# Performance work log

Hardware: AMD Instinct MI355X
Metric: run time of the kernel (lower is better)

## Reference

```python
import jax, jax.numpy as jnp
import numpy as np

N_HEAD, D_MODEL, D_HEAD = 16, 1024, 64
EPS = 1e-5
SCALE = 1.0 / np.sqrt(D_HEAD)


def setup_inputs() -> dict:
    key = jax.random.key(0)
    k1, k2, k3 = jax.random.split(key, 3)
    slen, bsz = 2048, 4
    h = jax.random.normal(k1, (slen, bsz, D_MODEL), dtype=jnp.float32)
    w_qkvb = jax.random.normal(k2, (N_HEAD * (3 * D_HEAD + 1), D_MODEL), dtype=jnp.float32) / np.sqrt(D_MODEL)
    w_o = jax.random.normal(k3, (D_MODEL, N_HEAD * D_HEAD), dtype=jnp.float32) / np.sqrt(N_HEAD * D_HEAD)
    ln_g = jnp.ones((D_MODEL,), dtype=jnp.float32)
    ln_b = jnp.zeros((D_MODEL,), dtype=jnp.float32)
    return {"h": h, "w_qkvb": w_qkvb, "w_o": w_o, "ln_g": ln_g, "ln_b": ln_b}


def _layer_norm(x, g, b):
    mu = jnp.mean(x, axis=-1, keepdims=True)
    var = jnp.mean(jnp.square(x - mu), axis=-1, keepdims=True)
    return (x - mu) * jax.lax.rsqrt(var + EPS) * g + b


def _fast_weight_memory(q, k, v, beta):
    # q,k,v: [b,h,l,d]; beta: [b,h,l,1]. Delta-rule recurrence over l.
    b, hn, l, d = q.shape
    qs = jnp.moveaxis(q, 2, 0)      # [l,b,h,d]
    ks = jnp.moveaxis(k, 2, 0)
    vs = jnp.moveaxis(v, 2, 0)
    bs = jnp.moveaxis(beta, 2, 0)   # [l,b,h,1]

    def step(W, xs):
        qt, kt, vt, bt = xs
        v_old = jnp.einsum('bhij,bhj->bhi', W, kt)
        delta = bt * (vt - v_old)                     # [b,h,d]
        W = W + delta[..., :, None] * kt[..., None, :]
        out = jnp.einsum('bhij,bhj->bhi', W, qt)
        return W, out

    W0 = jnp.zeros((b, hn, d, d), dtype=q.dtype)
    _, outs = jax.lax.scan(step, W0, (qs, ks, vs, bs))
    return jnp.moveaxis(outs, 0, 2)  # [b,h,l,d]


def reference(h, w_qkvb, w_o, ln_g, ln_b):
    slen, bsz, _ = h.shape
    qkvb = (h @ w_qkvb.T).reshape(slen, bsz, N_HEAD, 3 * D_HEAD + 1)
    q, k, v, beta = jnp.split(qkvb, [D_HEAD, 2 * D_HEAD, 3 * D_HEAD], axis=-1)
    beta = jax.nn.sigmoid(beta)
    # -> [b, h, l, d]
    q = jnp.transpose(q, (1, 2, 0, 3))
    k = jnp.transpose(k, (1, 2, 0, 3))
    v = jnp.transpose(v, (1, 2, 0, 3))
    beta = jnp.transpose(beta, (1, 2, 0, 3))

    q = jax.nn.elu(q) + 1.0
    k = jax.nn.elu(k) + 1.0
    k = k / jnp.sum(k, axis=-1, keepdims=True)
    q = q / jnp.sum(q, axis=-1, keepdims=True)

    denom_acc = jnp.cumsum(k, axis=2)  # [b,h,l,d]
    # key denominator: <cumsum(k)[t-1], k_t>, with t=0 forced to 1
    shifted = jnp.concatenate(
        [jnp.zeros_like(denom_acc[:, :, :1]), denom_acc[:, :, :-1]], axis=2)
    key_denom = jnp.einsum('bhld,bhld->bhl', shifted, k)
    key_denom = jnp.concatenate(
        [jnp.ones_like(key_denom[:, :, :1]), key_denom[:, :, 1:]], axis=2)[..., None]
    beta = beta * key_denom
    k = k / (key_denom + EPS)

    denominator = jnp.einsum('bhld,bhld->bhl', denom_acc, q)[..., None]

    layer_out = _fast_weight_memory(q, k, v, beta)
    layer_out = SCALE * layer_out / (denominator + EPS)  # [b,h,l,d]

    layer_out = jnp.transpose(layer_out, (0, 2, 1, 3)).reshape(
        layer_out.shape[0], slen, N_HEAD * D_HEAD)
    layer_out = jnp.transpose(layer_out, (1, 0, 2))  # [l,b,h*d]

    attn_out = layer_out @ w_o.T
    return _layer_norm(h + attn_out, ln_g, ln_b)
```

## Files before the change

### kernel.cpp

```cpp
#include <hip/hip_runtime.h>
#include <cstdint>
#include <cstddef>

#define D_HEAD   64
#define NHEAD    16
#define DMODEL   1024
#define SLEN     2048
#define BSZ      4
#define MROWS    (SLEN*BSZ)
#define NQKVB    (NHEAD*(3*D_HEAD+1))
#define NQPAD    3328
#define EPSV     1e-5f
#define SCALEV   0.125f
#define CHK      64
#define NCH      (SLEN/CHK)

typedef short bf16x8 __attribute__((ext_vector_type(8)));
typedef float f32x4  __attribute__((ext_vector_type(4)));

__device__ __forceinline__ unsigned short f2bf(float f){
  unsigned int u = __float_as_uint(f);
  u = (u + 0x7fffu + ((u >> 16) & 1u)) >> 16;
  return (unsigned short)u;
}
__device__ __forceinline__ float bf2f(unsigned short s){
  return __uint_as_float(((unsigned int)s) << 16);
}

__device__ __forceinline__ void gload_lds16(const unsigned short* g, unsigned short* l){
  __builtin_amdgcn_global_load_lds((const __attribute__((address_space(1))) void*)g,
                                   (__attribute__((address_space(3))) void*)l, 16, 0, 0);
}

#define SWZ(row, col) ((col) ^ (((row)&7)<<3))

__global__ void cast_bf16_kernel(const float* __restrict__ src,
                                 unsigned short* __restrict__ dst, int n4){
  int stride = gridDim.x * blockDim.x;
  for (int i = blockIdx.x*blockDim.x + threadIdx.x; i < n4; i += stride){
    float4 f = ((const float4*)src)[i];
    ushort4 u;
    u.x = f2bf(f.x); u.y = f2bf(f.y); u.z = f2bf(f.z); u.w = f2bf(f.w);
    ((ushort4*)dst)[i] = u;
  }
}

#define GBAR  do{ asm volatile("" ::: "memory"); __builtin_amdgcn_s_barrier(); asm volatile("" ::: "memory"); }while(0)
#define WVM2  asm volatile("s_waitcnt vmcnt(2)" ::: "memory")
#define WLG0  asm volatile("s_waitcnt lgkmcnt(0)" ::: "memory")
#define WLG8  asm volatile("s_waitcnt lgkmcnt(8)" ::: "memory")

#define LDA(sb_, mih_) do{ \
  _Pragma("unroll") \
  for (int m2 = 0; m2 < 4; ++m2) \
    _Pragma("unroll") \
    for (int ks = 0; ks < 2; ++ks) \
      aF[m2][ks] = frag(sb_, wmi*128 + (mih_)*64 + m2*16 + lm, ks); \
}while(0)

#define LDB(sb_, nih_) do{ \
  _Pragma("unroll") \
  for (int n2 = 0; n2 < 2; ++n2) \
    _Pragma("unroll") \
    for (int ks = 0; ks < 2; ++ks) \
      bF[(nih_)*2+n2][ks] = frag(sb_, wni*64 + (nih_)*32 + n2*16 + lm, ks); \
}while(0)

#define MMA(mih_, nih_) do{ \
  __builtin_amdgcn_s_setprio(1); \
  _Pragma("unroll") \
  for (int m2 = 0; m2 < 4; ++m2) \
    _Pragma("unroll") \
    for (int n2 = 0; n2 < 2; ++n2) \
      _Pragma("unroll") \
      for (int ks = 0; ks < 2; ++ks) \
        acc[(mih_)*4+m2][(nih_)*2+n2] = __builtin_amdgcn_mfma_f32_16x16x32_bf16( \
            aF[m2][ks], bF[(nih_)*2+n2][ks], acc[(mih_)*4+m2][(nih_)*2+n2], 0, 0, 0); \
  __builtin_amdgcn_s_setprio(0); \
}while(0)

template<bool OUT_BF16>
__global__ __launch_bounds__(512, 2) void gemm8p_kernel(
    const unsigned short* __restrict__ A, const unsigned short* __restrict__ B,
    void* __restrict__ C, int M, int N, int K, int tm){
  __shared__ __align__(16) unsigned short sA[2][256*64];
  __shared__ __align__(16) unsigned short sB[2][256*64];
  int tid = threadIdx.x;
  int wv = tid >> 6, ln = tid & 63, lm = ln & 15, quad = ln >> 4;
  int nwg = gridDim.x, wg = blockIdx.x;
  int cpx = nwg >> 3;
  int swzb = (wg & 7)*cpx + (wg >> 3);
  int bm = swzb % tm, bn = swzb / tm;
  int m0 = bm << 8, n0 = bn << 8;
  int wmi = wv >> 2, wni = wv & 3;
  const unsigned short* Ag = A + (size_t)m0*K;
  const unsigned short* Bg = B + (size_t)n0*K;

  f32x4 acc[8][4] = {};
  bf16x8 aF[4][2], bF[4][2];

  int e0 = wv*64 + ln;
  int r0row = e0 >> 3, r0cb = e0 & 7;
  int e1 = 512 + e0;
  int r1row = e1 >> 3, r1cb = e1 & 7;
  size_t gsrc0 = (size_t)r0row*K + ((r0cb ^ (r0row & 7)) << 3);
  size_t gsrc1 = (size_t)r1row*K + ((r1cb ^ (r1row & 7)) << 3);
  int ldst0 = (wv*64) * 8;
  int ldst1 = (512 + wv*64) * 8;

  auto stage = [&](const unsigned short* g, unsigned short* sb, int h, int kt){
    gload_lds16(g + (size_t)h*128*K + kt + gsrc0, sb + h*8192 + ldst0);
    gload_lds16(g + (size_t)h*128*K + kt + gsrc1, sb + h*8192 + ldst1);
  };
  auto frag = [&](const unsigned short* sb, int row, int ks)->bf16x8 {
    return *(const bf16x8*)(sb + row*64 + ((((ks<<2)+quad) ^ (row & 7)) << 3));
  };

  stage(Ag, sA[0], 0, 0);
  stage(Ag, sA[0], 1, 0);
  stage(Bg, sB[0], 0, 0);
  stage(Bg, sB[0], 1, 0);
  stage(Ag, sA[1], 0, 64);
  WVM2;
  GBAR;

  int nit = K >> 7;
  for (int i = 0; i < nit; ++i){
    int k1 = (i<<7) + 64;
    int k2 = ((i<<7) + 128) & (K-1);
    int k3 = ((i<<7) + 192) & (K-1);

    LDA(sA[0], 0); LDB(sB[0], 0);
    stage(Ag, sA[1], 1, k1);
    WLG8;
    GBAR; WLG0; MMA(0,0); GBAR;
    LDB(sB[0], 1);
    stage(Bg, sB[1], 0, k1);
    GBAR; WLG0; MMA(0,1); GBAR;
    LDA(sA[0], 1);
    stage(Bg, sB[1], 1, k1);
    GBAR; WLG0; MMA(1,0); GBAR;
    stage(Ag, sA[0], 0, k2);
    WVM2;
    GBAR; MMA(1,1); GBAR;
    LDA(sA[1], 0); LDB(sB[1], 0);
    stage(Ag, sA[0], 1, k2);
    WLG8;
    GBAR; WLG0; MMA(0,0); GBAR;
    LDB(sB[1], 1);
    stage(Bg, sB[0], 0, k2);
    GBAR; WLG0; MMA(0,1); GBAR;
    LDA(sA[1], 1);
    stage(Bg, sB[0], 1, k2);
    GBAR; WLG0; MMA(1,0); GBAR;
    stage(Ag, sA[1], 0, k3);
    WVM2;
    GBAR; MMA(1,1); GBAR;
  }
  asm volatile("s_waitcnt vmcnt(0)" ::: "memory");

  #pragma unroll
  for (int mi = 0; mi < 8; ++mi){
    int rowm = m0 + wmi*128 + mi*16 + quad*4;
    #pragma unroll
    for (int ni = 0; ni < 4; ++ni){
      int col = n0 + wni*64 + ni*16 + lm;
      size_t cb = (size_t)rowm * N + col;
      #pragma unroll
      for (int rr = 0; rr < 4; ++rr){
        float v = acc[mi][ni][rr];
        if (OUT_BF16) ((unsigned short*)C)[cb + (size_t)rr*N] = f2bf(v);
        else          ((float*)C)[cb + (size_t)rr*N] = v;
      }
    }
  }
  (void)M;
}

#undef LDA
#undef LDB
#undef MMA
#undef GBAR
#undef WVM2
#undef WLG0
#undef WLG8

__global__ __launch_bounds__(256) void prep_kernel(
    const unsigned short* __restrict__ qkvb,
    float* __restrict__ qb, float* __restrict__ kb,
    unsigned short* __restrict__ qb16, unsigned short* __restrict__ vb16,
    float4* __restrict__ scal){
  int gid = blockIdx.x*4 + (threadIdx.x >> 6);
  int ln  = threadIdx.x & 63;
  int m = gid >> 4, h = gid & 15;
  size_t rb = (size_t)m * NQPAD + (size_t)h * 193;
  float qr = bf2f(qkvb[rb + ln]);
  float kr = bf2f(qkvb[rb + 64 + ln]);
  float vr = bf2f(qkvb[rb + 128 + ln]);
  float br = bf2f(qkvb[rb + 192]);
  float q1 = qr > 0.f ? qr + 1.f : __expf(qr);
  float k1 = kr > 0.f ? kr + 1.f : __expf(kr);
  float sq = q1, sk = k1;
  #pragma unroll
  for (int off = 1; off < 64; off <<= 1){
    sq += __shfl_xor(sq, off, 64);
    sk += __shfl_xor(sk, off, 64);
  }
  float qn = q1 / sq, kn = k1 / sk;
  int b = m & 3, t = m >> 2;
  int bh = b*16 + h;
  size_t row = ((size_t)bh*SLEN + t)*64;
  qb[row + ln] = qn; kb[row + ln] = kn;
  qb16[row + SWZ(t, ln)] = f2bf(qn);
  vb16[row + ln] = f2bf(vr);
  if (ln == 0){
    float sb = 1.f / (1.f + __expf(-br));
    scal[(size_t)bh*SLEN + t] = make_float4(0.f, 0.f, 0.f, sb);
  }
}

#define NSEG 16
#define SEGL (SLEN/NSEG)
__global__ __launch_bounds__(64) void segsum_kernel(
    const float* __restrict__ kb, float* __restrict__ S){
  int bh = blockIdx.x, seg = blockIdx.y, ln = threadIdx.x;
  size_t base = ((size_t)bh*SLEN + (size_t)seg*SEGL)*64 + ln;
  float s = 0.f;
  #pragma unroll 4
  for (int t = 0; t < SEGL; ++t) s += kb[base + (size_t)t*64];
  S[((size_t)bh*NSEG + seg)*64 + ln] = s;
}
__global__ __launch_bounds__(64) void scan_kernel(
    const float* __restrict__ kb, const float* __restrict__ S,
    float* __restrict__ Ab){
  int bh = blockIdx.x, seg = blockIdx.y, ln = threadIdx.x;
  float acc = 0.f;
  for (int s = 0; s < seg; ++s) acc += S[((size_t)bh*NSEG + s)*64 + ln];
  size_t base = ((size_t)bh*SLEN + (size_t)seg*SEGL)*64 + ln;
  #pragma unroll 4
  for (int t = 0; t < SEGL; ++t){
    acc += kb[base + (size_t)t*64];
    Ab[base + (size_t)t*64] = acc;
  }
}

__global__ __launch_bounds__(256) void kden_kernel(
    const float* __restrict__ Ab, float* __restrict__ kb,
    const float* __restrict__ qb, unsigned short* __restrict__ kb16,
    float4* __restrict__ scal){
  int gid = blockIdx.x*4 + (threadIdx.x >> 6);
  int ln  = threadIdx.x & 63;
  int t = gid & (SLEN-1);
  size_t o = (size_t)gid*64 + ln;
  float a = Ab[o], kn = kb[o], qn = qb[o];
  float d0 = (a - kn)*kn, d1 = a*qn, d2 = kn*qn;
  #pragma unroll
  for (int off = 1; off < 64; off <<= 1){
    d0 += __shfl_xor(d0, off, 64);
    d1 += __shfl_xor(d1, off, 64);
    d2 += __shfl_xor(d2, off, 64);
  }
  float kd  = (t == 0) ? 1.f : d0;
  float inv = 1.f / (kd + EPSV);
  float kf = kn * inv;
  kb[o] = kf;
  kb16[(size_t)gid*64 + SWZ(t, ln)] = f2bf(kf);
  if (ln == 0){
    float4 s = scal[gid];
    scal[gid] = make_float4(s.w * kd, d2 * inv, SCALEV/(d1 + EPSV), 0.f);
  }
}

__global__ __launch_bounds__(64, 1) void precomp_kernel(
    const unsigned short* __restrict__ K16, const unsigned short* __restrict__ Q16,
    const float4* __restrict__ scal,
    unsigned short* __restrict__ Dg, unsigned short* __restrict__ Bg){
  __shared__ __align__(16) float sA[64*64];
  __shared__ float sbp[64];
  int inst = blockIdx.x;
  int bh = inst >> 5, ch = inst & 31;
  int ln = threadIdx.x, lm = ln & 15, quad = ln >> 4;
  const unsigned short* Kg = K16 + ((size_t)bh*SLEN + ch*CHK)*64;
  const unsigned short* Qg = Q16 + ((size_t)bh*SLEN + ch*CHK)*64;

  {
    f32x4 acc[4][4] = {};
    #pragma unroll
    for (int s = 0; s < 2; ++s){
      bf16x8 kf[4];
      #pragma unroll
      for (int i = 0; i < 4; ++i){
        int row = i*16+lm;
        kf[i] = *(const bf16x8*)(Kg + (size_t)row*64 + SWZ(row, s*32 + quad*8));
      }
      #pragma unroll
      for (int mi = 0; mi < 4; ++mi)
        #pragma unroll
        for (int ni = 0; ni < 4; ++ni)
          acc[mi][ni] = __builtin_amdgcn_mfma_f32_16x16x32_bf16(kf[mi], kf[ni], acc[mi][ni], 0, 0, 0);
    }
    #pragma unroll
    for (int mi = 0; mi < 4; ++mi)
      #pragma unroll
      for (int ni = 0; ni < 4; ++ni)
        #pragma unroll
        for (int rr = 0; rr < 4; ++rr)
          sA[(mi*16+quad*4+rr)*64 + ni*16+lm] = acc[mi][ni][rr];
  }
  sbp[ln] = scal[(size_t)bh*SLEN + ch*CHK + ln].x;
  __syncthreads();

  {
    f32x4 acc[4][4] = {};
    #pragma unroll
    for (int s = 0; s < 2; ++s){
      bf16x8 kf[4], qf[4];
      #pragma unroll
      for (int i = 0; i < 4; ++i){
        int row = i*16+lm;
        kf[i] = *(const bf16x8*)(Kg + (size_t)row*64 + SWZ(row, s*32 + quad*8));
        qf[i] = *(const bf16x8*)(Qg + (size_t)row*64 + SWZ(row, s*32 + quad*8));
      }
      #pragma unroll
      for (int mi = 0; mi < 4; ++mi)
        #pragma unroll
        for (int ni = 0; ni < 4; ++ni)
          acc[mi][ni] = __builtin_amdgcn_mfma_f32_16x16x32_bf16(qf[mi], kf[ni], acc[mi][ni], 0, 0, 0);
    }
    size_t io = (size_t)inst*4096;
    #pragma unroll
    for (int mi = 0; mi < 4; ++mi)
      #pragma unroll
      for (int ni = 0; ni < 4; ++ni)
        #pragma unroll
        for (int rr = 0; rr < 4; ++rr){
          int t = mi*16+quad*4+rr, j = ni*16+lm;
          float v = (j <= t) ? acc[mi][ni][rr] : 0.f;
          Bg[io + (size_t)t*64 + SWZ(t, j)] = f2bf(v);
        }
  }

  {
    float x[64];
    x[0] = (ln == 0) ? sbp[0] : 0.f;
    #pragma unroll
    for (int i = 1; i < 64; ++i){
      float bi = sbp[i];
      float s = 0.f;
      #pragma unroll
      for (int m4 = 0; m4*4 < i; ++m4){
        float4 a = *(const float4*)&sA[i*64 + m4*4];
        if (m4*4+0 < i) s += a.x * x[m4*4+0];
        if (m4*4+1 < i) s += a.y * x[m4*4+1];
        if (m4*4+2 < i) s += a.z * x[m4*4+2];
        if (m4*4+3 < i) s += a.w * x[m4*4+3];
      }
      x[i] = ((ln == i) ? bi : 0.f) - bi*s;
    }
    size_t io = (size_t)inst*4096;
    #pragma unroll
    for (int i = 0; i < 64; ++i)
      Dg[io + (size_t)i*64 + SWZ(i, ln)] = f2bf(x[i]);
  }
}

__global__ __launch_bounds__(256, 1) void chunk_kernel(
    const unsigned short* __restrict__ K16, const unsigned short* __restrict__ Q16,
    const unsigned short* __restrict__ V16,
    const unsigned short* __restrict__ Dg, const unsigned short* __restrict__ Bg,
    const float4* __restrict__ scal, unsigned short* __restrict__ lo){
  __shared__ __align__(16) unsigned short sK[4096];
  __shared__ __align__(16) unsigned short sQ[4096];
  __shared__ __align__(16) unsigned short sD[4096];
  __shared__ __align__(16) unsigned short sB[4096];
  __shared__ __align__(16) unsigned short sKT[4096];
  __shared__ __align__(16) unsigned short sV[1024];
  __shared__ __align__(16) unsigned short sX[1024];
  __shared__ __align__(16) unsigned short sDT[1024];
  __shared__ __align__(16) unsigned short sW[1024];
  int bh = blockIdx.x, rg = blockIdx.y;
  int tid = threadIdx.x, wv = tid >> 6, ln = tid & 63, lm = ln & 15, quad = ln >> 4;
  size_t sb = (size_t)bh*SLEN*64;
  const unsigned short* Kg = K16 + sb;
  const unsigned short* Qg = Q16 + sb;
  const unsigned short* Vg = V16 + sb;
  const float4* scp = scal + (size_t)bh*SLEN;
  size_t lobase = (size_t)(bh>>4)*DMODEL + (size_t)(bh&15)*64 + rg*16;

  auto dma8 = [&](const unsigned short* g, unsigned short* s){
    #pragma unroll
    for (int it = 0; it < 2; ++it)
      gload_lds16(g + (wv*2+it)*512 + ln*8, s + (wv*2+it)*512);
  };
  auto dma_chunk = [&](int ch){
    size_t co = (size_t)ch*CHK*64;
    dma8(Kg + co, sK);
    dma8(Qg + co, sQ);
    size_t io = ((size_t)bh*NCH + ch)*4096;
    dma8(Dg + io, sD);
    dma8(Bg + io, sB);
    if (wv == 0){
      gload_lds16(Vg + co + (size_t)(ln>>1)*64 + rg*16 + (ln&1)*8, sV);
      gload_lds16(Vg + co + (size_t)(32 + (ln>>1))*64 + rg*16 + (ln&1)*8, sV + 512);
    }
  };
  auto frag = [&](const unsigned short* S, int row, int kb)->bf16x8 {
    return *(const bf16x8*)(S + row*64 + SWZ(row, kb));
  };

  if (tid < 128) ((uint4*)sW)[tid] = make_uint4(0u,0u,0u,0u);
  f32x4 Wacc = {0,0,0,0};
  dma_chunk(0);

  for (int ch = 0; ch < NCH; ++ch){
    int tb = ch*CHK + wv*16 + quad*4;
    float sz0 = scp[tb+0].z, sz1 = scp[tb+1].z, sz2 = scp[tb+2].z, sz3 = scp[tb+3].z;
    __builtin_amdgcn_s_waitcnt(0x0F70);
    __syncthreads();

    f32x4 Macc = {0,0,0,0}, Mqacc = {0,0,0,0};
    #pragma unroll
    for (int s = 0; s < 2; ++s){
      int kb = s*32 + quad*8;
      bf16x8 ak = frag(sK, wv*16+lm, kb);
      bf16x8 aq = frag(sQ, wv*16+lm, kb);
      bf16x8 bw = frag(sW, lm, kb);
      Macc  = __builtin_amdgcn_mfma_f32_16x16x32_bf16(ak, bw, Macc, 0, 0, 0);
      Mqacc = __builtin_amdgcn_mfma_f32_16x16x32_bf16(aq, bw, Mqacc, 0, 0, 0);
    }
    int d0 = wv*16;
    uint4 kr0 = *(const uint4*)(sK + ln*64 + SWZ(ln, d0));
    uint4 kr1 = *(const uint4*)(sK + ln*64 + SWZ(ln, d0+8));
    #pragma unroll
    for (int rr = 0; rr < 4; ++rr){
      int t = wv*16 + quad*4 + rr;
      float x = bf2f(sV[t*16 + lm]) - Macc[rr];
      sX[lm*64 + SWZ(lm, t)] = f2bf(x);
    }
    {
      const unsigned short* k0p = (const unsigned short*)&kr0;
      const unsigned short* k1p = (const unsigned short*)&kr1;
      #pragma unroll
      for (int e = 0; e < 8; ++e){
        int d = d0 + e;
        sKT[d*64 + SWZ(d, ln)] = k0p[e];
      }
      #pragma unroll
      for (int e = 0; e < 8; ++e){
        int d = d0 + 8 + e;
        sKT[d*64 + SWZ(d, ln)] = k1p[e];
      }
    }
    __syncthreads();

    f32x4 Dacc = {0,0,0,0};
    #pragma unroll
    for (int s = 0; s < 2; ++s){
      int kb = s*32 + quad*8;
      bf16x8 ad = frag(sD, wv*16+lm, kb);
      bf16x8 bx = frag(sX, lm, kb);
      Dacc = __builtin_amdgcn_mfma_f32_16x16x32_bf16(ad, bx, Dacc, 0, 0, 0);
    }
    #pragma unroll
    for (int rr = 0; rr < 4; ++rr){
      int t = wv*16 + quad*4 + rr;
      sDT[lm*64 + SWZ(lm, t)] = f2bf(Dacc[rr]);
    }
    __syncthreads();

    f32x4 Oacc = Mqacc;
    #pragma unroll
    for (int s = 0; s < 2; ++s){
      int kb = s*32 + quad*8;
      bf16x8 ab = frag(sB, wv*16+lm, kb);
      bf16x8 bd = frag(sDT, lm, kb);
      Oacc = __builtin_amdgcn_mfma_f32_16x16x32_bf16(ab, bd, Oacc, 0, 0, 0);
      bf16x8 adt = frag(sDT, lm, kb);
      bf16x8 bkt = frag(sKT, wv*16+lm, kb);
      Wacc = __builtin_amdgcn_mfma_f32_16x16x32_bf16(adt, bkt, Wacc, 0, 0, 0);
    }
    #pragma unroll
    for (int rr = 0; rr < 4; ++rr){
      int tabs = ch*CHK + wv*16 + quad*4 + rr;
      float sz = (rr==0)?sz0:(rr==1)?sz1:(rr==2)?sz2:sz3;
      lo[lobase + (size_t)tabs*(BSZ*DMODEL) + lm] = f2bf(Oacc[rr] * sz);
    }
    __syncthreads();

    if (ch + 1 < NCH) dma_chunk(ch + 1);
    #pragma unroll
    for (int rr = 0; rr < 4; ++rr){
      int r = quad*4 + rr, d = wv*16 + lm;
      sW[r*64 + SWZ(r, d)] = f2bf(Wacc[rr]);
    }
  }
}

__global__ __launch_bounds__(256) void ln_kernel(
    const float* __restrict__ hin, const float* __restrict__ attn,
    const float* __restrict__ g, const float* __restrict__ bta,
    float* __restrict__ out){
  int row = blockIdx.x, tid = threadIdx.x;
  size_t rb = (size_t)row * DMODEL;
  float4 hv = ((const float4*)(hin + rb))[tid];
  float4 av = ((const float4*)(attn + rb))[tid];
  float4 x;
  x.x = hv.x + av.x; x.y = hv.y + av.y; x.z = hv.z + av.z; x.w = hv.w + av.w;
  float s  = x.x + x.y + x.z + x.w;
  float ss = x.x*x.x + x.y*x.y + x.z*x.z + x.w*x.w;
  #pragma unroll
  for (int off = 1; off < 64; off <<= 1){
    s  += __shfl_xor(s , off, 64);
    ss += __shfl_xor(ss, off, 64);
  }
  __shared__ float ls[4], lq[4];
  int wv = tid >> 6, ln = tid & 63;
  if (ln == 0){ ls[wv] = s; lq[wv] = ss; }
  __syncthreads();
  s  = ls[0] + ls[1] + ls[2] + ls[3];
  ss = lq[0] + lq[1] + lq[2] + lq[3];
  float mu  = s * (1.f/DMODEL);
  float var = ss * (1.f/DMODEL) - mu*mu;
  float rstd = rsqrtf(var + EPSV);
  float4 gv = ((const float4*)g)[tid], bv = ((const float4*)bta)[tid];
  float4 o;
  o.x = (x.x-mu)*rstd*gv.x + bv.x;
  o.y = (x.y-mu)*rstd*gv.y + bv.y;
  o.z = (x.z-mu)*rstd*gv.z + bv.z;
  o.w = (x.w-mu)*rstd*gv.w + bv.w;
  ((float4*)(out + rb))[tid] = o;
}

extern "C" void kernel_launch(void* const* d_in, const int* in_sizes, int n_in,
                              void* d_out, int out_size, void* d_ws, size_t ws_size,
                              hipStream_t stream){
  const float* h     = (const float*)d_in[0];
  const float* wqkvb = (const float*)d_in[1];
  const float* wo    = (const float*)d_in[2];
  const float* lng   = (const float*)d_in[3];
  const float* lnb   = (const float*)d_in[4];
  float* out = (float*)d_out;

  char* w = (char*)d_ws;
  auto take = [&](size_t bytes)->char*{
    char* p = w; w += (bytes + 255) & ~(size_t)255; return p;
  };
  unsigned short* h_bf    = (unsigned short*)take((size_t)MROWS*DMODEL*2);
  unsigned short* wq_bf   = (unsigned short*)take((size_t)NQPAD*DMODEL*2);
  unsigned short* wo_bf   = (unsigned short*)take((size_t)DMODEL*DMODEL*2);
  unsigned short* qkvb_bf = (unsigned short*)take((size_t)MROWS*NQPAD*2);
  float* qb   = (float*)take((size_t)MROWS*DMODEL*4 + 4096);
  float* kb   = (float*)take((size_t)MROWS*DMODEL*4 + 4096);
  float* Ab   = (float*)take((size_t)MROWS*DMODEL*4);
  float4* scal = (float4*)take((size_t)64*SLEN*16 + 4096);
  unsigned short* lo_bf = (unsigned short*)take((size_t)MROWS*DMODEL*2);
  float* Sseg = (float*)take((size_t)64*NSEG*64*4);
  unsigned short* kb16 = (unsigned short*)take((size_t)MROWS*DMODEL*2);
  unsigned short* qb16 = (unsigned short*)take((size_t)MROWS*DMODEL*2);
  unsigned short* vb16 = (unsigned short*)take((size_t)MROWS*DMODEL*2);
  unsigned short* Dg = (unsigned short*)Ab;
  unsigned short* Bg = (unsigned short*)Ab + (size_t)64*NCH*4096;
  float* attn = Ab;

  cast_bf16_kernel<<<2048, 256, 0, stream>>>(h,     h_bf,  MROWS*DMODEL/4);
  cast_bf16_kernel<<<1024, 256, 0, stream>>>(wqkvb, wq_bf, NQKVB*DMODEL/4);
  cast_bf16_kernel<<<512,  256, 0, stream>>>(wo,    wo_bf, DMODEL*DMODEL/4);

  gemm8p_kernel<true><<<(MROWS/256)*(NQPAD/256), 512, 0, stream>>>(
      h_bf, wq_bf, qkvb_bf, MROWS, NQPAD, DMODEL, MROWS/256);

  prep_kernel<<<MROWS*NHEAD/4, 256, 0, stream>>>(qkvb_bf, qb, kb, qb16, vb16, scal);
  segsum_kernel<<<dim3(64, NSEG), 64, 0, stream>>>(kb, Sseg);
  scan_kernel<<<dim3(64, NSEG), 64, 0, stream>>>(kb, Sseg, Ab);
  kden_kernel<<<64*SLEN/4, 256, 0, stream>>>(Ab, kb, qb, kb16, scal);
  precomp_kernel<<<64*NCH, 64, 0, stream>>>(kb16, qb16, scal, Dg, Bg);
  chunk_kernel<<<dim3(64, 4), 256, 0, stream>>>(kb16, qb16, vb16, Dg, Bg, scal, lo_bf);

  gemm8p_kernel<false><<<(MROWS/256)*(DMODEL/256), 512, 0, stream>>>(
      lo_bf, wo_bf, attn, MROWS, DMODEL, DMODEL, MROWS/256);

  ln_kernel<<<MROWS, 256, 0, stream>>>(h, attn, lng, lnb, out);
  (void)in_sizes; (void)n_in; (void)out_size; (void)ws_size;
}
```

Baseline: 395.9 us.

## Fuse casts and scan/kden, double-buffer chunk kernel, split-K output GEMM

Merges the three bf16 cast launches into one kernel and folds the cumulative-sum scan into the key-denominator computation, so the Ab intermediate is never written and re-read. The chunk kernel now double-buffers its LDS tiles and prefetches the next chunk right after the barrier, removing one __syncthreads per chunk. The output projection GEMM uses a 2-way split-K to double its workgroup count, with the two partial results summed inside the layernorm kernel. The GEMM's vmcnt wait is also moved after the last MMA. The trade-offs are extra LDS in the chunk kernel, an additional fp32 partial buffer that the layernorm must read, and a per-token shuffle reduction inside the serial scan loop.

```diff
diff --git a/kernel.cpp b/kernel.cpp
--- a/kernel.cpp
+++ b/kernel.cpp
@@ -34,14 +34,20 @@
 
 #define SWZ(row, col) ((col) ^ (((row)&7)<<3))
 
-__global__ void cast_bf16_kernel(const float* __restrict__ src,
-                                 unsigned short* __restrict__ dst, int n4){
+__global__ void cast3_kernel(const float* __restrict__ s0, unsigned short* __restrict__ d0, int n0,
+                             const float* __restrict__ s1, unsigned short* __restrict__ d1, int n1,
+                             const float* __restrict__ s2, unsigned short* __restrict__ d2, int n2){
+  int total = n0 + n1 + n2;
   int stride = gridDim.x * blockDim.x;
-  for (int i = blockIdx.x*blockDim.x + threadIdx.x; i < n4; i += stride){
-    float4 f = ((const float4*)src)[i];
+  for (int i = blockIdx.x*blockDim.x + threadIdx.x; i < total; i += stride){
+    const float* s; unsigned short* d; int j = i;
+    if (j < n0){ s = s0; d = d0; }
+    else if (j < n0 + n1){ j -= n0; s = s1; d = d1; }
+    else { j -= n0 + n1; s = s2; d = d2; }
+    float4 f = ((const float4*)s)[j];
     ushort4 u;
     u.x = f2bf(f.x); u.y = f2bf(f.y); u.z = f2bf(f.z); u.w = f2bf(f.w);
-    ((ushort4*)dst)[i] = u;
+    ((ushort4*)d)[j] = u;
   }
 }
 
@@ -79,10 +85,10 @@
   __builtin_amdgcn_s_setprio(0); \
 }while(0)
 
-template<bool OUT_BF16>
+template<bool OUT_BF16, bool SPLITK>
 __global__ __launch_bounds__(512, 2) void gemm8p_kernel(
     const unsigned short* __restrict__ A, const unsigned short* __restrict__ B,
-    void* __restrict__ C, int M, int N, int K, int tm){
+    void* __restrict__ C, void* __restrict__ C2, int N, int K, int lda, int tm){
   __shared__ __align__(16) unsigned short sA[2][256*64];
   __shared__ __align__(16) unsigned short sB[2][256*64];
   int tid = threadIdx.x;
@@ -90,11 +96,13 @@
   int nwg = gridDim.x, wg = blockIdx.x;
   int cpx = nwg >> 3;
   int swzb = (wg & 7)*cpx + (wg >> 3);
+  int kh = 0;
+  if (SPLITK){ int half = nwg >> 1; if (swzb >= half){ kh = 1; swzb -= half; } }
   int bm = swzb % tm, bn = swzb / tm;
   int m0 = bm << 8, n0 = bn << 8;
   int wmi = wv >> 2, wni = wv & 3;
-  const unsigned short* Ag = A + (size_t)m0*K;
-  const unsigned short* Bg = B + (size_t)n0*K;
+  const unsigned short* Ag = A + (size_t)m0*lda + (size_t)kh*K;
+  const unsigned short* Bg = B + (size_t)n0*lda + (size_t)kh*K;
 
   f32x4 acc[8][4] = {};
   bf16x8 aF[4][2], bF[4][2];
@@ -103,14 +111,14 @@
   int r0row = e0 >> 3, r0cb = e0 & 7;
   int e1 = 512 + e0;
   int r1row = e1 >> 3, r1cb = e1 & 7;
-  size_t gsrc0 = (size_t)r0row*K + ((r0cb ^ (r0row & 7)) << 3);
-  size_t gsrc1 = (size_t)r1row*K + ((r1cb ^ (r1row & 7)) << 3);
+  size_t gsrc0 = (size_t)r0row*lda + ((r0cb ^ (r0row & 7)) << 3);
+  size_t gsrc1 = (size_t)r1row*lda + ((r1cb ^ (r1row & 7)) << 3);
   int ldst0 = (wv*64) * 8;
   int ldst1 = (512 + wv*64) * 8;
 
   auto stage = [&](const unsigned short* g, unsigned short* sb, int h, int kt){
-    gload_lds16(g + (size_t)h*128*K + kt + gsrc0, sb + h*8192 + ldst0);
-    gload_lds16(g + (size_t)h*128*K + kt + gsrc1, sb + h*8192 + ldst1);
+    gload_lds16(g + (size_t)h*128*lda + kt + gsrc0, sb + h*8192 + ldst0);
+    gload_lds16(g + (size_t)h*128*lda + kt + gsrc1, sb + h*8192 + ldst1);
   };
   auto frag = [&](const unsigned short* sb, int row, int ks)->bf16x8 {
     return *(const bf16x8*)(sb + row*64 + ((((ks<<2)+quad) ^ (row & 7)) << 3));
@@ -141,8 +149,7 @@
     stage(Bg, sB[1], 1, k1);
     GBAR; WLG0; MMA(1,0); GBAR;
     stage(Ag, sA[0], 0, k2);
-    WVM2;
-    GBAR; MMA(1,1); GBAR;
+    GBAR; MMA(1,1); WVM2; GBAR;
     LDA(sA[1], 0); LDB(sB[1], 0);
     stage(Ag, sA[0], 1, k2);
     WLG8;
@@ -154,11 +161,11 @@
     stage(Bg, sB[0], 1, k2);
     GBAR; WLG0; MMA(1,0); GBAR;
     stage(Ag, sA[1], 0, k3);
-    WVM2;
-    GBAR; MMA(1,1); GBAR;
+    GBAR; MMA(1,1); WVM2; GBAR;
   }
   asm volatile("s_waitcnt vmcnt(0)" ::: "memory");
 
+  float* Cf = (float*)((SPLITK && kh) ? C2 : C);
   #pragma unroll
   for (int mi = 0; mi < 8; ++mi){
     int rowm = m0 + wmi*128 + mi*16 + quad*4;
@@ -170,11 +177,10 @@
       for (int rr = 0; rr < 4; ++rr){
         float v = acc[mi][ni][rr];
         if (OUT_BF16) ((unsigned short*)C)[cb + (size_t)rr*N] = f2bf(v);
-        else          ((float*)C)[cb + (size_t)rr*N] = v;
+        else          Cf[cb + (size_t)rr*N] = v;
       }
     }
   }
-  (void)M;
 }
 
 #undef LDA
@@ -230,44 +236,39 @@
   for (int t = 0; t < SEGL; ++t) s += kb[base + (size_t)t*64];
   S[((size_t)bh*NSEG + seg)*64 + ln] = s;
 }
-__global__ __launch_bounds__(64) void scan_kernel(
-    const float* __restrict__ kb, const float* __restrict__ S,
-    float* __restrict__ Ab){
+
+__global__ __launch_bounds__(64) void scan_kden_kernel(
+    const float* __restrict__ kb, const float* __restrict__ qb,
+    const float* __restrict__ S, unsigned short* __restrict__ kb16,
+    float4* __restrict__ scal){
   int bh = blockIdx.x, seg = blockIdx.y, ln = threadIdx.x;
   float acc = 0.f;
   for (int s = 0; s < seg; ++s) acc += S[((size_t)bh*NSEG + s)*64 + ln];
   size_t base = ((size_t)bh*SLEN + (size_t)seg*SEGL)*64 + ln;
-  #pragma unroll 4
-  for (int t = 0; t < SEGL; ++t){
-    acc += kb[base + (size_t)t*64];
-    Ab[base + (size_t)t*64] = acc;
-  }
-}
-
-__global__ __launch_bounds__(256) void kden_kernel(
-    const float* __restrict__ Ab, float* __restrict__ kb,
-    const float* __restrict__ qb, unsigned short* __restrict__ kb16,
-    float4* __restrict__ scal){
-  int gid = blockIdx.x*4 + (threadIdx.x >> 6);
-  int ln  = threadIdx.x & 63;
-  int t = gid & (SLEN-1);
-  size_t o = (size_t)gid*64 + ln;
-  float a = Ab[o], kn = kb[o], qn = qb[o];
-  float d0 = (a - kn)*kn, d1 = a*qn, d2 = kn*qn;
-  #pragma unroll
-  for (int off = 1; off < 64; off <<= 1){
-    d0 += __shfl_xor(d0, off, 64);
-    d1 += __shfl_xor(d1, off, 64);
-    d2 += __shfl_xor(d2, off, 64);
-  }
-  float kd  = (t == 0) ? 1.f : d0;
-  float inv = 1.f / (kd + EPSV);
-  float kf = kn * inv;
-  kb[o] = kf;
-  kb16[(size_t)gid*64 + SWZ(t, ln)] = f2bf(kf);
-  if (ln == 0){
-    float4 s = scal[gid];
-    scal[gid] = make_float4(s.w * kd, d2 * inv, SCALEV/(d1 + EPSV), 0.f);
+  int t0 = seg*SEGL;
+  #pragma unroll 2
+  for (int i = 0; i < SEGL; ++i){
+    size_t o = base + (size_t)i*64;
+    float kn = kb[o], qn = qb[o];
+    acc += kn;
+    float a = acc;
+    float d0 = (a - kn)*kn, d1 = a*qn, d2 = kn*qn;
+    #pragma unroll
+    for (int off = 1; off < 64; off <<= 1){
+      d0 += __shfl_xor(d0, off, 64);
+      d1 += __shfl_xor(d1, off, 64);
+      d2 += __shfl_xor(d2, off, 64);
+    }
+    int t = t0 + i;
+    float kd  = (t == 0) ? 1.f : d0;
+    float inv = 1.f / (kd + EPSV);
+    float kf = kn * inv;
+    int gid = bh*SLEN + t;
+    kb16[(size_t)gid*64 + SWZ(t, ln)] = f2bf(kf);
+    if (ln == 0){
+      float4 sc = scal[gid];
+      scal[gid] = make_float4(sc.w * kd, d2 * inv, SCALEV/(d1 + EPSV), 0.f);
+    }
   }
 }
 
@@ -369,12 +370,12 @@
     const unsigned short* __restrict__ V16,
     const unsigned short* __restrict__ Dg, const unsigned short* __restrict__ Bg,
     const float4* __restrict__ scal, unsigned short* __restrict__ lo){
-  __shared__ __align__(16) unsigned short sK[4096];
-  __shared__ __align__(16) unsigned short sQ[4096];
-  __shared__ __align__(16) unsigned short sD[4096];
-  __shared__ __align__(16) unsigned short sB[4096];
+  __shared__ __align__(16) unsigned short sK[2][4096];
+  __shared__ __align__(16) unsigned short sQ[2][4096];
+  __shared__ __align__(16) unsigned short sD[2][4096];
+  __shared__ __align__(16) unsigned short sB[2][4096];
+  __shared__ __align__(16) unsigned short sV[2][1024];
   __shared__ __align__(16) unsigned short sKT[4096];
-  __shared__ __align__(16) unsigned short sV[1024];
   __shared__ __align__(16) unsigned short sX[1024];
   __shared__ __align__(16) unsigned short sDT[1024];
   __shared__ __align__(16) unsigned short sW[1024];
@@ -392,16 +393,16 @@
     for (int it = 0; it < 2; ++it)
       gload_lds16(g + (wv*2+it)*512 + ln*8, s + (wv*2+it)*512);
   };
-  auto dma_chunk = [&](int ch){
+  auto dma_chunk = [&](int ch, int p){
     size_t co = (size_t)ch*CHK*64;
-    dma8(Kg + co, sK);
-    dma8(Qg + co, sQ);
+    dma8(Kg + co, sK[p]);
+    dma8(Qg + co, sQ[p]);
     size_t io = ((size_t)bh*NCH + ch)*4096;
-    dma8(Dg + io, sD);
-    dma8(Bg + io, sB);
+    dma8(Dg + io, sD[p]);
+    dma8(Bg + io, sB[p]);
     if (wv == 0){
-      gload_lds16(Vg + co + (size_t)(ln>>1)*64 + rg*16 + (ln&1)*8, sV);
-      gload_lds16(Vg + co + (size_t)(32 + (ln>>1))*64 + rg*16 + (ln&1)*8, sV + 512);
+      gload_lds16(Vg + co + (size_t)(ln>>1)*64 + rg*16 + (ln&1)*8, sV[p]);
+      gload_lds16(Vg + co + (size_t)(32 + (ln>>1))*64 + rg*16 + (ln&1)*8, sV[p] + 512);
     }
   };
   auto frag = [&](const unsigned short* S, int row, int kb)->bf16x8 {
@@ -410,31 +411,38 @@
 
   if (tid < 128) ((uint4*)sW)[tid] = make_uint4(0u,0u,0u,0u);
   f32x4 Wacc = {0,0,0,0};
-  dma_chunk(0);
+  dma_chunk(0, 0);
 
   for (int ch = 0; ch < NCH; ++ch){
+    int p = ch & 1;
+    const unsigned short* cK = sK[p];
+    const unsigned short* cQ = sQ[p];
+    const unsigned short* cD = sD[p];
+    const unsigned short* cB = sB[p];
+    const unsigned short* cV = sV[p];
     int tb = ch*CHK + wv*16 + quad*4;
     float sz0 = scp[tb+0].z, sz1 = scp[tb+1].z, sz2 = scp[tb+2].z, sz3 = scp[tb+3].z;
     __builtin_amdgcn_s_waitcnt(0x0F70);
     __syncthreads();
+    if (ch + 1 < NCH) dma_chunk(ch + 1, p ^ 1);
 
     f32x4 Macc = {0,0,0,0}, Mqacc = {0,0,0,0};
     #pragma unroll
     for (int s = 0; s < 2; ++s){
       int kb = s*32 + quad*8;
-      bf16x8 ak = frag(sK, wv*16+lm, kb);
-      bf16x8 aq = frag(sQ, wv*16+lm, kb);
+      bf16x8 ak = frag(cK, wv*16+lm, kb);
+      bf16x8 aq = frag(cQ, wv*16+lm, kb);
       bf16x8 bw = frag(sW, lm, kb);
       Macc  = __builtin_amdgcn_mfma_f32_16x16x32_bf16(ak, bw, Macc, 0, 0, 0);
       Mqacc = __builtin_amdgcn_mfma_f32_16x16x32_bf16(aq, bw, Mqacc, 0, 0, 0);
     }
     int d0 = wv*16;
-    uint4 kr0 = *(const uint4*)(sK + ln*64 + SWZ(ln, d0));
-    uint4 kr1 = *(const uint4*)(sK + ln*64 + SWZ(ln, d0+8));
+    uint4 kr0 = *(const uint4*)(cK + ln*64 + SWZ(ln, d0));
+    uint4 kr1 = *(const uint4*)(cK + ln*64 + SWZ(ln, d0+8));
     #pragma unroll
     for (int rr = 0; rr < 4; ++rr){
       int t = wv*16 + quad*4 + rr;
-      float x = bf2f(sV[t*16 + lm]) - Macc[rr];
+      float x = bf2f(cV[t*16 + lm]) - Macc[rr];
       sX[lm*64 + SWZ(lm, t)] = f2bf(x);
     }
     {
@@ -457,7 +465,7 @@
     #pragma unroll
     for (int s = 0; s < 2; ++s){
       int kb = s*32 + quad*8;
-      bf16x8 ad = frag(sD, wv*16+lm, kb);
+      bf16x8 ad = frag(cD, wv*16+lm, kb);
       bf16x8 bx = frag(sX, lm, kb);
       Dacc = __builtin_amdgcn_mfma_f32_16x16x32_bf16(ad, bx, Dacc, 0, 0, 0);
     }
@@ -472,7 +480,7 @@
     #pragma unroll
     for (int s = 0; s < 2; ++s){
       int kb = s*32 + quad*8;
-      bf16x8 ab = frag(sB, wv*16+lm, kb);
+      bf16x8 ab = frag(cB, wv*16+lm, kb);
       bf16x8 bd = frag(sDT, lm, kb);
       Oacc = __builtin_amdgcn_mfma_f32_16x16x32_bf16(ab, bd, Oacc, 0, 0, 0);
       bf16x8 adt = frag(sDT, lm, kb);
@@ -485,9 +493,6 @@
       float sz = (rr==0)?sz0:(rr==1)?sz1:(rr==2)?sz2:sz3;
       lo[lobase + (size_t)tabs*(BSZ*DMODEL) + lm] = f2bf(Oacc[rr] * sz);
     }
-    __syncthreads();
-
-    if (ch + 1 < NCH) dma_chunk(ch + 1);
     #pragma unroll
     for (int rr = 0; rr < 4; ++rr){
       int r = quad*4 + rr, d = wv*16 + lm;
@@ -497,15 +502,18 @@
 }
 
 __global__ __launch_bounds__(256) void ln_kernel(
-    const float* __restrict__ hin, const float* __restrict__ attn,
+    const float* __restrict__ hin, const float* __restrict__ a0,
+    const float* __restrict__ a1,
     const float* __restrict__ g, const float* __restrict__ bta,
     float* __restrict__ out){
   int row = blockIdx.x, tid = threadIdx.x;
   size_t rb = (size_t)row * DMODEL;
   float4 hv = ((const float4*)(hin + rb))[tid];
-  float4 av = ((const float4*)(attn + rb))[tid];
+  float4 v0 = ((const float4*)(a0 + rb))[tid];
+  float4 v1 = ((const float4*)(a1 + rb))[tid];
   float4 x;
-  x.x = hv.x + av.x; x.y = hv.y + av.y; x.z = hv.z + av.z; x.w = hv.w + av.w;
+  x.x = hv.x + v0.x + v1.x; x.y = hv.y + v0.y + v1.y;
+  x.z = hv.z + v0.z + v1.z; x.w = hv.w + v0.w + v1.w;
   float s  = x.x + x.y + x.z + x.w;
   float ss = x.x*x.x + x.y*x.y + x.z*x.z + x.w*x.w;
   #pragma unroll
@@ -560,25 +568,25 @@
   unsigned short* vb16 = (unsigned short*)take((size_t)MROWS*DMODEL*2);
   unsigned short* Dg = (unsigned short*)Ab;
   unsigned short* Bg = (unsigned short*)Ab + (size_t)64*NCH*4096;
-  float* attn = Ab;
-
-  cast_bf16_kernel<<<2048, 256, 0, stream>>>(h,     h_bf,  MROWS*DMODEL/4);
-  cast_bf16_kernel<<<1024, 256, 0, stream>>>(wqkvb, wq_bf, NQKVB*DMODEL/4);
-  cast_bf16_kernel<<<512,  256, 0, stream>>>(wo,    wo_bf, DMODEL*DMODEL/4);
-
-  gemm8p_kernel<true><<<(MROWS/256)*(NQPAD/256), 512, 0, stream>>>(
-      h_bf, wq_bf, qkvb_bf, MROWS, NQPAD, DMODEL, MROWS/256);
+  float* attn0 = Ab;
+  float* attn1 = qb;
+
+  cast3_kernel<<<2048, 256, 0, stream>>>(h, h_bf, MROWS*DMODEL/4,
+                                         wqkvb, wq_bf, NQKVB*DMODEL/4,
+                                         wo, wo_bf, DMODEL*DMODEL/4);
+
+  gemm8p_kernel<true, false><<<(MROWS/256)*(NQPAD/256), 512, 0, stream>>>(
+      h_bf, wq_bf, qkvb_bf, nullptr, NQPAD, DMODEL, DMODEL, MROWS/256);
 
   prep_kernel<<<MROWS*NHEAD/4, 256, 0, stream>>>(qkvb_bf, qb, kb, qb16, vb16, scal);
   segsum_kernel<<<dim3(64, NSEG), 64, 0, stream>>>(kb, Sseg);
-  scan_kernel<<<dim3(64, NSEG), 64, 0, stream>>>(kb, Sseg, Ab);
-  kden_kernel<<<64*SLEN/4, 256, 0, stream>>>(Ab, kb, qb, kb16, scal);
+  scan_kden_kernel<<<dim3(64, NSEG), 64, 0, stream>>>(kb, qb, Sseg, kb16, scal);
   precomp_kernel<<<64*NCH, 64, 0, stream>>>(kb16, qb16, scal, Dg, Bg);
   chunk_kernel<<<dim3(64, 4), 256, 0, stream>>>(kb16, qb16, vb16, Dg, Bg, scal, lo_bf);
 
-  gemm8p_kernel<false><<<(MROWS/256)*(DMODEL/256), 512, 0, stream>>>(
-      lo_bf, wo_bf, attn, MROWS, DMODEL, DMODEL, MROWS/256);
-
-  ln_kernel<<<MROWS, 256, 0, stream>>>(h, attn, lng, lnb, out);
+  gemm8p_kernel<false, true><<<2*(MROWS/256)*(DMODEL/256), 512, 0, stream>>>(
+      lo_bf, wo_bf, attn0, attn1, DMODEL, DMODEL/2, DMODEL, MROWS/256);
+
+  ln_kernel<<<MROWS, 256, 0, stream>>>(h, attn0, attn1, lng, lnb, out);
   (void)in_sizes; (void)n_in; (void)out_size; (void)ws_size;
 }
```

New measurement: 432.2 us. 9.2% more time.
